# Performance work log

Hardware: AMD Instinct MI355X
Metric: run time of the kernel (lower is better)

Reference implementation:

```python
import jax, jax.numpy as jnp
import numpy as np

KB = 0.0019872041      # Boltzmann constant, kcal/(mol*K)
TEMP = 300.0
ALPHA = 10.0
BW = 0.15              # Gaussian KDE bandwidth
PAIR_I = jnp.array([0, 0, 0, 1, 1, 2])
PAIR_J = jnp.array([1, 2, 3, 2, 3, 3])

B, N_ATOMS = 512, 1024
G, L, K, D = 256, 8, 128, 6


def setup_inputs() -> dict:
    key = jax.random.key(0)
    k1, k2, k3, k4, k5, k6 = jax.random.split(key, 6)
    positions = jax.random.normal(k1, (B, N_ATOMS, 3), dtype=jnp.float32) * 2.0
    # KDE training samples live in 6-dim distance space (positive, few Angstroms)
    kde_samples = jax.random.uniform(k2, (G, L, K, D), dtype=jnp.float32) * 5.0
    weight = jax.random.uniform(k3, (G, L), dtype=jnp.float32)
    offset = jax.random.normal(k4, (G, L), dtype=jnp.float32)
    atom_idxs = jax.random.randint(k5, (G, L, 4), 0, N_ATOMS)
    group_sizes = jax.random.randint(k6, (G,), 0, L)  # clamped to >=1 in reference
    return {"positions": positions, "kde_samples": kde_samples, "weight": weight,
            "offset": offset, "atom_idxs": atom_idxs, "group_sizes": group_sizes}


def reference(positions, kde_samples, weight, offset, atom_idxs, group_sizes):
    Gn, Ln, Kn, Dn = kde_samples.shape
    # Gather the 4 vertices of every loss: [B, G, L, 4, 3]
    vp = positions[:, atom_idxs]
    # 6 pairwise distances per loss: [B, G, L, 6]
    diff = vp[..., PAIR_I, :] - vp[..., PAIR_J, :]
    dists = jnp.sqrt(jnp.sum(diff * diff, axis=-1) + 1e-12)
    # Gaussian KDE log-density over the K training samples, expanded squared
    x2 = jnp.sum(dists * dists, axis=-1)          # [B,G,L]
    mu2 = jnp.sum(kde_samples * kde_samples, -1)  # [G,L,K]
    xmu = jnp.einsum('bgld,glkd->bglk', dists, kde_samples)
    sq = x2[..., None] + mu2[None] - 2.0 * xmu    # [B,G,L,K]
    log_norm = jnp.log(jnp.float32(Kn)) + 0.5 * Dn * jnp.log(2.0 * jnp.pi * BW * BW)
    logP = jax.nn.logsumexp(-sq / (2.0 * BW * BW), axis=-1) - log_norm  # [B,G,L]
    energy = -KB * TEMP * logP
    scaled = energy * weight + offset             # [B,G,L]
    # Ragged group reduction: min over the valid losses of each group
    sizes = jnp.maximum(group_sizes, 1)
    mask = jnp.arange(Ln)[None, :] < sizes[:, None]        # [G,L]
    group_min = jnp.min(jnp.where(mask, scaled, jnp.inf), axis=-1)  # [B,G]
    # soft-min across groups
    return -jax.nn.logsumexp(-ALPHA * group_min, axis=-1) / ALPHA   # [B]
```

## Files before the change

### kernel.cpp

```cpp
#include <hip/hip_runtime.h>

#define NB 512
#define NATOMS 1024
#define NG 256
#define NL 8
#define NK 128

#define KBT 0.59616123f
#define ALPHA_C 10.0f
#define LN2 0.6931471805599453f
#define LOG2E 1.4426950408889634f
#define INV2BW2 22.222221f
#define SCALE2 (INV2BW2 * LOG2E)
#define LOG_NORM (-1.0170649f)

#define WL_CAP 2048
#define FILL_BLOCKS 128

typedef _Float16 f16x8 __attribute__((ext_vector_type(8)));
typedef float f32x16 __attribute__((ext_vector_type(16)));

__device__ __forceinline__ float fexp2(float x) { return __builtin_amdgcn_exp2f(x); }
__device__ __forceinline__ float flog2(float x) { return __builtin_amdgcn_logf(x); }

__device__ __forceinline__ unsigned fkey(float f) {
  unsigned u = __float_as_uint(f);
  return (u & 0x80000000u) ? ~u : (u | 0x80000000u);
}
__device__ __forceinline__ float funkey(unsigned k) {
  unsigned u = (k & 0x80000000u) ? (k ^ 0x80000000u) : ~k;
  return __uint_as_float(u);
}

__device__ __forceinline__ float wred_min(float v) {
#pragma unroll
  for (int m = 32; m >= 1; m >>= 1) v = fminf(v, __shfl_xor(v, m, 64));
  return v;
}
__device__ __forceinline__ float wred_sum(float v) {
#pragma unroll
  for (int m = 32; m >= 1; m >>= 1) v += __shfl_xor(v, m, 64);
  return v;
}

__global__ __launch_bounds__(256) void prep_all(
    const float* __restrict__ kde, const int* __restrict__ gsizes,
    int* __restrict__ wl, uint4* __restrict__ gmin_u4,
    f16x8* __restrict__ tabA) {
  const int t = threadIdx.x;
  const int bid = blockIdx.x;

  if (bid == 0) {
    const int lane = t & 63, wid = t >> 6;
    int gs = gsizes[t];
    int nl = gs < 1 ? 1 : (gs > NL ? NL : gs);
    int x = nl;
#pragma unroll
    for (int m = 1; m < 64; m <<= 1) {
      int y = __shfl_up(x, m, 64);
      if (lane >= m) x += y;
    }
    __shared__ int wsum[4];
    if (lane == 63) wsum[wid] = x;
    __syncthreads();
    int off = 0;
    for (int i = 0; i < wid; ++i) off += wsum[i];
    int inc = off + x, exc = inc - nl;
    for (int j = 0; j < nl; ++j) wl[exc + j] = (t << 3) | j;
    if (t == 255) wl[WL_CAP] = inc;
    return;
  }
  if (bid <= FILL_BLOCKS) {
    const unsigned F = 0xFFFFFFFFu;
    gmin_u4[(bid - 1) * 256 + t] = make_uint4(F, F, F, F);
    return;
  }

  const int gl = (bid - 129) * 4 + (t >> 6);
  const int l = t & 63;
  const int m = l & 31, h = l >> 5;
#pragma unroll
  for (int kt = 0; kt < 4; ++kt) {
    const int k = kt * 32 + m;
    const float* mp = kde + ((size_t)gl * NK + k) * 6;
    float mu2 = 0.0f;
    _Float16 ah[6], al[6];
#pragma unroll
    for (int q = 0; q < 6; ++q) {
      float mv = mp[q];
      mu2 += mv * mv;
      float a = (2.0f * SCALE2) * mv;
      _Float16 hh = (_Float16)a;
      ah[q] = hh;
      al[q] = (_Float16)(a - (float)hh);
    }
    float z = -SCALE2 * mu2;
    _Float16 z1 = (_Float16)z;
    _Float16 z2 = (_Float16)(z - (float)z1);
    const _Float16 Z = (_Float16)0.0f;
    f16x8 j0 = (h == 0)
      ? (f16x8){ah[0],ah[1],ah[2],ah[3],ah[4],ah[5],al[0],al[1]}
      : (f16x8){al[2],al[3],al[4],al[5],ah[0],ah[1],ah[2],ah[3]};
    f16x8 j1 = (h == 0)
      ? (f16x8){ah[4],ah[5],al[0],al[1],al[2],al[3],al[4],al[5]}
      : (f16x8){z1,  z2,  Z,   Z,   Z,   Z,   Z,   Z   };
    const size_t base = ((size_t)gl * 4 + kt) * 2;
    tabA[(base + 0) * 64 + l] = j0;
    tabA[(base + 1) * 64 + l] = j1;
  }
}

__global__ __launch_bounds__(256) void stage1_kernel(
    const float* __restrict__ positions, const f16x8* __restrict__ tabA,
    const float* __restrict__ weight, const float* __restrict__ offs,
    const int* __restrict__ atom_idxs, const int* __restrict__ wl,
    unsigned* __restrict__ gmin_u) {
  const int count = wl[WL_CAP];
  const int w = blockIdx.x >> 2;
  if (w >= count) return;
  const int gl = wl[w];
  const int g = gl >> 3;

  const int t = threadIdx.x;
  const int lane = t & 63;
  const int col = lane & 31, h = lane >> 5;
  const int b = ((blockIdx.x & 3) << 7) + ((t >> 6) << 5) + col;

  const int4 idx = *reinterpret_cast<const int4*>(atom_idxs + (gl << 2));
  const int ids[4] = {idx.x, idx.y, idx.z, idx.w};
  const float* pb = positions + (size_t)b * NATOMS * 3;
  float ax[4], ay[4], az[4];
#pragma unroll
  for (int j = 0; j < 4; ++j) {
    const float3 p = *reinterpret_cast<const float3*>(pb + ids[j] * 3);
    ax[j] = p.x; ay[j] = p.y; az[j] = p.z;
  }
  const int PI_[6] = {0, 0, 0, 1, 1, 2};
  const int PJ_[6] = {1, 2, 3, 2, 3, 3};
  float d[6]; float x2 = 0.0f;
#pragma unroll
  for (int q = 0; q < 6; ++q) {
    float dx = ax[PI_[q]] - ax[PJ_[q]];
    float dy = ay[PI_[q]] - ay[PJ_[q]];
    float dz = az[PI_[q]] - az[PJ_[q]];
    float dd = dx * dx + dy * dy + dz * dz + 1e-12f;
    d[q] = sqrtf(dd);
    x2 += d[q] * d[q];
  }
  const float c2 = -x2 * SCALE2;

  _Float16 xh[6], xl[6];
#pragma unroll
  for (int q = 0; q < 6; ++q) {
    _Float16 hh = (_Float16)d[q];
    xh[q] = hh;
    xl[q] = (_Float16)(d[q] - (float)hh);
  }
  const _Float16 ONE = (_Float16)1.0f, Z = (_Float16)0.0f;
  f16x8 Bf0 = (h == 0)
    ? (f16x8){xh[0],xh[1],xh[2],xh[3],xh[4],xh[5],xh[0],xh[1]}
    : (f16x8){xh[2],xh[3],xh[4],xh[5],xl[0],xl[1],xl[2],xl[3]};
  f16x8 Bf1 = (h == 0)
    ? (f16x8){xl[4],xl[5],xl[0],xl[1],xl[2],xl[3],xl[4],xl[5]}
    : (f16x8){ONE,  ONE,  Z,   Z,   Z,   Z,   Z,   Z   };

  const f16x8* tp = tabA + (size_t)gl * 8 * 64 + lane;
  const f32x16 zz = {0.0f};
  f32x16 acc[4];
#pragma unroll
  for (int kt = 0; kt < 4; ++kt) {
    f16x8 A0 = tp[(kt * 2 + 0) * 64];
    f16x8 A1 = tp[(kt * 2 + 1) * 64];
    acc[kt] = __builtin_amdgcn_mfma_f32_32x32x16_f16(
        A1, Bf1, __builtin_amdgcn_mfma_f32_32x32x16_f16(A0, Bf0, zz, 0, 0, 0),
        0, 0, 0);
  }

  float mkt[4];
#pragma unroll
  for (int kt = 0; kt < 4; ++kt) {
    float m0 = fmaxf(fmaxf(acc[kt][0], acc[kt][1]), fmaxf(acc[kt][2], acc[kt][3]));
    float m1 = fmaxf(fmaxf(acc[kt][4], acc[kt][5]), fmaxf(acc[kt][6], acc[kt][7]));
    float m2 = fmaxf(fmaxf(acc[kt][8], acc[kt][9]), fmaxf(acc[kt][10], acc[kt][11]));
    float m3 = fmaxf(fmaxf(acc[kt][12], acc[kt][13]), fmaxf(acc[kt][14], acc[kt][15]));
    mkt[kt] = fmaxf(fmaxf(m0, m1), fmaxf(m2, m3));
  }
  float mx = fmaxf(fmaxf(mkt[0], mkt[1]), fmaxf(mkt[2], mkt[3]));
  mx = fmaxf(mx, __shfl_xor(mx, 32, 64));

  float s0 = 0.0f, s1 = 0.0f, s2 = 0.0f, s3 = 0.0f;
#pragma unroll
  for (int kt = 0; kt < 4; ++kt) {
    s0 += fexp2(acc[kt][0] - mx)  + fexp2(acc[kt][1] - mx)
        + fexp2(acc[kt][2] - mx)  + fexp2(acc[kt][3] - mx);
    s1 += fexp2(acc[kt][4] - mx)  + fexp2(acc[kt][5] - mx)
        + fexp2(acc[kt][6] - mx)  + fexp2(acc[kt][7] - mx);
    s2 += fexp2(acc[kt][8] - mx)  + fexp2(acc[kt][9] - mx)
        + fexp2(acc[kt][10] - mx) + fexp2(acc[kt][11] - mx);
    s3 += fexp2(acc[kt][12] - mx) + fexp2(acc[kt][13] - mx)
        + fexp2(acc[kt][14] - mx) + fexp2(acc[kt][15] - mx);
  }
  float s = (s0 + s1) + (s2 + s3);
  s += __shfl_xor(s, 32, 64);

  if (h == 0) {
    float lse2 = c2 + mx + flog2(s);
    float logP = lse2 * LN2 - LOG_NORM;
    float scaled = -KBT * logP * weight[gl] + offs[gl];
    atomicMin(&gmin_u[g * NB + b], fkey(scaled));
  }
}

__global__ __launch_bounds__(256) void stage2_kernel(
    const unsigned* __restrict__ gmin_u, float* __restrict__ out) {
  const int b = blockIdx.x;
  const int t = threadIdx.x;
  const int lane = t & 63;
  const int wid = t >> 6;
  float v = funkey(gmin_u[t * NB + b]);
  __shared__ float sm[4], ss[4];
  float m = wred_min(v);
  if (lane == 0) sm[wid] = m;
  __syncthreads();
  float M = fminf(fminf(sm[0], sm[1]), fminf(sm[2], sm[3]));
  float e = fexp2(-ALPHA_C * LOG2E * (v - M));
  float s = wred_sum(e);
  if (lane == 0) ss[wid] = s;
  __syncthreads();
  if (t == 0) {
    float S = ss[0] + ss[1] + ss[2] + ss[3];
    out[b] = M - flog2(S) * LN2 / ALPHA_C;
  }
}

extern "C" void kernel_launch(void* const* d_in, const int* in_sizes, int n_in,
                              void* d_out, int out_size, void* d_ws, size_t ws_size,
                              hipStream_t stream) {
  const float* positions = (const float*)d_in[0];
  const float* kde       = (const float*)d_in[1];
  const float* weight    = (const float*)d_in[2];
  const float* offs      = (const float*)d_in[3];
  const int*   atom_idxs = (const int*)d_in[4];
  const int*   gsizes    = (const int*)d_in[5];
  float* out = (float*)d_out;

  unsigned* gmin_u = (unsigned*)d_ws;
  int* wl = (int*)d_ws + (size_t)NG * NB;
  f16x8* tabA = (f16x8*)((char*)d_ws + (1 << 20));

  prep_all<<<dim3(1 + FILL_BLOCKS + 512), dim3(256), 0, stream>>>(
      kde, gsizes, wl, (uint4*)gmin_u, tabA);
  stage1_kernel<<<dim3(WL_CAP * 4), dim3(256), 0, stream>>>(
      positions, tabA, weight, offs, atom_idxs, wl, gmin_u);
  stage2_kernel<<<dim3(NB), dim3(256), 0, stream>>>(gmin_u, out);
}
```

Baseline: 39.32 us.

## Fuse KDE table preparation into stage1 via shared memory

Moves the fp16 split-precision KDE table construction out of the prep kernel and into stage1, where the first 128 threads build the per-loss table in LDS before the MFMA loop. This removes the 512 table-building blocks and the global round trip through the tabA workspace. In exchange, each stage1 block (four per loss) recomputes the table, and a block-wide barrier now sits before the MFMAs.

```diff
diff --git a/kernel.cpp b/kernel.cpp
--- a/kernel.cpp
+++ b/kernel.cpp
@@ -43,46 +43,64 @@
   return v;
 }
 
-__global__ __launch_bounds__(256) void prep_all(
-    const float* __restrict__ kde, const int* __restrict__ gsizes,
-    int* __restrict__ wl, uint4* __restrict__ gmin_u4,
-    f16x8* __restrict__ tabA) {
+__global__ __launch_bounds__(256) void prep_small(
+    const int* __restrict__ gsizes, int* __restrict__ wl,
+    uint4* __restrict__ gmin_u4) {
   const int t = threadIdx.x;
-  const int bid = blockIdx.x;
-
-  if (bid == 0) {
-    const int lane = t & 63, wid = t >> 6;
-    int gs = gsizes[t];
-    int nl = gs < 1 ? 1 : (gs > NL ? NL : gs);
-    int x = nl;
-#pragma unroll
-    for (int m = 1; m < 64; m <<= 1) {
-      int y = __shfl_up(x, m, 64);
-      if (lane >= m) x += y;
-    }
-    __shared__ int wsum[4];
-    if (lane == 63) wsum[wid] = x;
-    __syncthreads();
-    int off = 0;
-    for (int i = 0; i < wid; ++i) off += wsum[i];
-    int inc = off + x, exc = inc - nl;
-    for (int j = 0; j < nl; ++j) wl[exc + j] = (t << 3) | j;
-    if (t == 255) wl[WL_CAP] = inc;
+  if (blockIdx.x != 0) {
+    const unsigned F = 0xFFFFFFFFu;
+    gmin_u4[(blockIdx.x - 1) * 256 + t] = make_uint4(F, F, F, F);
     return;
   }
-  if (bid <= FILL_BLOCKS) {
-    const unsigned F = 0xFFFFFFFFu;
-    gmin_u4[(bid - 1) * 256 + t] = make_uint4(F, F, F, F);
-    return;
-  }
-
-  const int gl = (bid - 129) * 4 + (t >> 6);
-  const int l = t & 63;
-  const int m = l & 31, h = l >> 5;
-#pragma unroll
-  for (int kt = 0; kt < 4; ++kt) {
-    const int k = kt * 32 + m;
-    const float* mp = kde + ((size_t)gl * NK + k) * 6;
+  const int lane = t & 63, wid = t >> 6;
+  int gs = gsizes[t];
+  int nl = gs < 1 ? 1 : (gs > NL ? NL : gs);
+  int x = nl;
+#pragma unroll
+  for (int m = 1; m < 64; m <<= 1) {
+    int y = __shfl_up(x, m, 64);
+    if (lane >= m) x += y;
+  }
+  __shared__ int wsum[4];
+  if (lane == 63) wsum[wid] = x;
+  __syncthreads();
+  int off = 0;
+  for (int i = 0; i < wid; ++i) off += wsum[i];
+  int inc = off + x, exc = inc - nl;
+  for (int j = 0; j < nl; ++j) wl[exc + j] = (t << 3) | j;
+  if (t == 255) wl[WL_CAP] = inc;
+}
+
+__global__ __launch_bounds__(256) void stage1_kernel(
+    const float* __restrict__ positions, const float* __restrict__ kde,
+    const float* __restrict__ weight, const float* __restrict__ offs,
+    const int* __restrict__ atom_idxs, const int* __restrict__ wl,
+    unsigned* __restrict__ gmin_u) {
+  const int count = wl[WL_CAP];
+  const int w = blockIdx.x >> 2;
+  if (w >= count) return;
+  const int gl = wl[w];
+  const int g = gl >> 3;
+
+  const int t = threadIdx.x;
+  const int lane = t & 63;
+  const int col = lane & 31, h = lane >> 5;
+  const int b = ((blockIdx.x & 3) << 7) + ((t >> 6) << 5) + col;
+
+  __shared__ f16x8 tabL[8][64];
+
+  const int4 idx = *reinterpret_cast<const int4*>(atom_idxs + (gl << 2));
+  const int ids[4] = {idx.x, idx.y, idx.z, idx.w};
+  const float* pb = positions + (size_t)b * NATOMS * 3;
+  float ax[4], ay[4], az[4];
+#pragma unroll
+  for (int j = 0; j < 4; ++j) {
+    const float3 p = *reinterpret_cast<const float3*>(pb + ids[j] * 3);
+    ax[j] = p.x; ay[j] = p.y; az[j] = p.z;
+  }
+
+  if (t < NK) {
+    const float* mp = kde + ((size_t)gl * NK + t) * 6;
     float mu2 = 0.0f;
     _Float16 ah[6], al[6];
 #pragma unroll
@@ -98,43 +116,13 @@
     _Float16 z1 = (_Float16)z;
     _Float16 z2 = (_Float16)(z - (float)z1);
     const _Float16 Z = (_Float16)0.0f;
-    f16x8 j0 = (h == 0)
-      ? (f16x8){ah[0],ah[1],ah[2],ah[3],ah[4],ah[5],al[0],al[1]}
-      : (f16x8){al[2],al[3],al[4],al[5],ah[0],ah[1],ah[2],ah[3]};
-    f16x8 j1 = (h == 0)
-      ? (f16x8){ah[4],ah[5],al[0],al[1],al[2],al[3],al[4],al[5]}
-      : (f16x8){z1,  z2,  Z,   Z,   Z,   Z,   Z,   Z   };
-    const size_t base = ((size_t)gl * 4 + kt) * 2;
-    tabA[(base + 0) * 64 + l] = j0;
-    tabA[(base + 1) * 64 + l] = j1;
-  }
-}
-
-__global__ __launch_bounds__(256) void stage1_kernel(
-    const float* __restrict__ positions, const f16x8* __restrict__ tabA,
-    const float* __restrict__ weight, const float* __restrict__ offs,
-    const int* __restrict__ atom_idxs, const int* __restrict__ wl,
-    unsigned* __restrict__ gmin_u) {
-  const int count = wl[WL_CAP];
-  const int w = blockIdx.x >> 2;
-  if (w >= count) return;
-  const int gl = wl[w];
-  const int g = gl >> 3;
-
-  const int t = threadIdx.x;
-  const int lane = t & 63;
-  const int col = lane & 31, h = lane >> 5;
-  const int b = ((blockIdx.x & 3) << 7) + ((t >> 6) << 5) + col;
-
-  const int4 idx = *reinterpret_cast<const int4*>(atom_idxs + (gl << 2));
-  const int ids[4] = {idx.x, idx.y, idx.z, idx.w};
-  const float* pb = positions + (size_t)b * NATOMS * 3;
-  float ax[4], ay[4], az[4];
-#pragma unroll
-  for (int j = 0; j < 4; ++j) {
-    const float3 p = *reinterpret_cast<const float3*>(pb + ids[j] * 3);
-    ax[j] = p.x; ay[j] = p.y; az[j] = p.z;
-  }
+    const int kt = t >> 5, m = t & 31;
+    tabL[kt * 2 + 0][m]      = (f16x8){ah[0],ah[1],ah[2],ah[3],ah[4],ah[5],al[0],al[1]};
+    tabL[kt * 2 + 0][m + 32] = (f16x8){al[2],al[3],al[4],al[5],ah[0],ah[1],ah[2],ah[3]};
+    tabL[kt * 2 + 1][m]      = (f16x8){ah[4],ah[5],al[0],al[1],al[2],al[3],al[4],al[5]};
+    tabL[kt * 2 + 1][m + 32] = (f16x8){z1,  z2,  Z,   Z,   Z,   Z,   Z,   Z   };
+  }
+
   const int PI_[6] = {0, 0, 0, 1, 1, 2};
   const int PJ_[6] = {1, 2, 3, 2, 3, 3};
   float d[6]; float x2 = 0.0f;
@@ -164,13 +152,14 @@
     ? (f16x8){xl[4],xl[5],xl[0],xl[1],xl[2],xl[3],xl[4],xl[5]}
     : (f16x8){ONE,  ONE,  Z,   Z,   Z,   Z,   Z,   Z   };
 
-  const f16x8* tp = tabA + (size_t)gl * 8 * 64 + lane;
+  __syncthreads();
+
   const f32x16 zz = {0.0f};
   f32x16 acc[4];
 #pragma unroll
   for (int kt = 0; kt < 4; ++kt) {
-    f16x8 A0 = tp[(kt * 2 + 0) * 64];
-    f16x8 A1 = tp[(kt * 2 + 1) * 64];
+    f16x8 A0 = tabL[kt * 2 + 0][lane];
+    f16x8 A1 = tabL[kt * 2 + 1][lane];
     acc[kt] = __builtin_amdgcn_mfma_f32_32x32x16_f16(
         A1, Bf1, __builtin_amdgcn_mfma_f32_32x32x16_f16(A0, Bf0, zz, 0, 0, 0),
         0, 0, 0);
@@ -246,11 +235,10 @@
 
   unsigned* gmin_u = (unsigned*)d_ws;
   int* wl = (int*)d_ws + (size_t)NG * NB;
-  f16x8* tabA = (f16x8*)((char*)d_ws + (1 << 20));
-
-  prep_all<<<dim3(1 + FILL_BLOCKS + 512), dim3(256), 0, stream>>>(
-      kde, gsizes, wl, (uint4*)gmin_u, tabA);
+
+  prep_small<<<dim3(1 + FILL_BLOCKS), dim3(256), 0, stream>>>(
+      gsizes, wl, (uint4*)gmin_u);
   stage1_kernel<<<dim3(WL_CAP * 4), dim3(256), 0, stream>>>(
-      positions, tabA, weight, offs, atom_idxs, wl, gmin_u);
+      positions, kde, weight, offs, atom_idxs, wl, gmin_u);
   stage2_kernel<<<dim3(NB), dim3(256), 0, stream>>>(gmin_u, out);
 }
```

New measurement: 35.85 us. 8.8% less time.
